# Performance work log

Measured on AMD Instinct MI355X. Metric: run time of the kernel, lower is better.

Reference implementation:

```python
import jax, jax.numpy as jnp
import numpy as np

N_STREAMS = 8
DIM = 1024
N_HEADS = 16
HEAD_DIM = DIM // N_HEADS
STREAM_DIM = DIM // N_STREAMS
EPS = 1e-6


def setup_inputs() -> dict:
    key = jax.random.key(0)
    ks = jax.random.split(key, 20)
    B, S, D = 2, 2048, DIM
    inp = {
        "x": jax.random.normal(ks[0], (B, S, D), jnp.float32),
        "rope_cos": jax.random.uniform(ks[1], (S, HEAD_DIM), jnp.float32),
        "rope_sin": jax.random.uniform(ks[2], (S, HEAD_DIM), jnp.float32),
        # DeltaOperator: learned per-channel decay logits
        "delta_decay": jax.random.normal(ks[3], (D,), jnp.float32) * 0.02,
        # gate_proj: Linear(D, 3*n)
        "gate_w": jax.random.normal(ks[4], (3 * N_STREAMS, D), jnp.float32) * 0.02,
        "gate_b": jnp.zeros((3 * N_STREAMS,), jnp.float32),
        "phi_res": jax.random.normal(ks[5], (N_STREAMS, N_STREAMS), jnp.float32) * 0.02,
        "ln1_w": jnp.ones((D,), jnp.float32),
        "ln2_w": jnp.ones((D,), jnp.float32),
        # MLP (StrategicLinear == Linear at inference)
        "w1": jax.random.normal(ks[6], (4 * D, D), jnp.float32) * 0.02,
        "b1": jnp.zeros((4 * D,), jnp.float32),
        "w2": jax.random.normal(ks[7], (D, 4 * D), jnp.float32) * 0.02,
        "b2": jnp.zeros((D,), jnp.float32),
        # nn.MultiheadAttention params
        "in_proj_w": jax.random.normal(ks[8], (3 * D, D), jnp.float32) * 0.02,
        "in_proj_b": jnp.zeros((3 * D,), jnp.float32),
        "out_w": jax.random.normal(ks[9], (D, D), jnp.float32) * 0.02,
        "out_b": jnp.zeros((D,), jnp.float32),
    }
    return inp


def delta_operator(x, decay_logits):
    # out_t = x_t - s_{t-1};  s_t = beta*s_{t-1} + (1-beta)*x_t  (per-channel EMA delta)
    beta = jax.nn.sigmoid(decay_logits)  # [D]

    def step(s, xt):
        out = xt - s
        s_new = beta * s + (1.0 - beta) * xt
        return s_new, out

    xT = jnp.swapaxes(x, 0, 1)  # [S,B,D]
    s0 = jnp.zeros_like(xT[0])
    _, ysT = jax.lax.scan(step, s0, xT)
    return jnp.swapaxes(ysT, 0, 1)  # [B,S,D]


def rms_norm(x, w):
    var = jnp.mean(x * x, axis=-1, keepdims=True)
    return x * jax.lax.rsqrt(var + EPS) * w


def sinkhorn_knopp(phi, iterations=15):
    K = jnp.exp(phi)
    for _ in range(iterations):
        K = K / jnp.sum(K, axis=1, keepdims=True)
        K = K / jnp.sum(K, axis=0, keepdims=True)
    return K


def causal_mha(x, in_proj_w, in_proj_b, out_w, out_b):
    B, S, D = x.shape
    qkv = x @ in_proj_w.T + in_proj_b  # [B,S,3D]
    q, k, v = jnp.split(qkv, 3, axis=-1)
    def heads(t):
        return t.reshape(B, S, N_HEADS, HEAD_DIM).transpose(0, 2, 1, 3)  # [B,H,S,hd]
    q, k, v = heads(q), heads(k), heads(v)
    scores = jnp.einsum("bhqd,bhkd->bhqk", q, k) / jnp.sqrt(jnp.float32(HEAD_DIM))
    mask = jnp.tril(jnp.ones((S, S), bool))
    scores = jnp.where(mask, scores, jnp.float32(-1e9))
    attn = jax.nn.softmax(scores, axis=-1)
    o = jnp.einsum("bhqk,bhkd->bhqd", attn, v)
    o = o.transpose(0, 2, 1, 3).reshape(B, S, D)
    return o @ out_w.T + out_b


def reference(x, rope_cos, rope_sin, delta_decay, gate_w, gate_b, phi_res,
              ln1_w, ln2_w, w1, b1, w2, b2, in_proj_w, in_proj_b, out_w, out_b):
    B, S, D = x.shape
    n = N_STREAMS
    x_delta = delta_operator(x, delta_decay)
    x_state = jnp.mean(x_delta, axis=1)  # [B,D]
    gates = x_state @ gate_w.T + gate_b  # [B,3n]
    g_res = jax.nn.sigmoid(gates[:, 2 * n:])[:, None, :, None]  # [B,1,n,1]
    H_res = sinkhorn_knopp(phi_res, 15)
    x_streams = x_delta.reshape(B, S, n, STREAM_DIM)
    # (x_perm @ H.T).permute back == einsum over stream axis
    mhc_out = jnp.einsum("bsnd,mn->bsmd", x_streams * g_res, H_res).reshape(B, S, D)
    normed = rms_norm(x_delta, ln1_w)
    attn_out = causal_mha(normed, in_proj_w, in_proj_b, out_w, out_b)
    normed2 = rms_norm(x_delta + attn_out, ln2_w)
    h = jax.nn.gelu(normed2 @ w1.T + b1, approximate=False)
    ffn_out = h @ w2.T + b2
    return x_delta + attn_out + ffn_out + mhc_out
```

## Files before the change

### kernel.cpp

```cpp
#include <hip/hip_runtime.h>
#include <hip/hip_bf16.h>
#include <math.h>

#define BB 2
#define SS 2048
#define DDIM 1024
#define NHEAD 16
#define NSTR 8
#define SDIMC 128
#define NCH 16
#define CLEN 128
#define EPSV 1e-6f

using bf16 = __hip_bfloat16;
typedef __attribute__((ext_vector_type(8))) __bf16 bf8;
typedef __attribute__((ext_vector_type(4))) __bf16 bf4v;
typedef __attribute__((ext_vector_type(4))) float f4;

__device__ __forceinline__ bf16 f2b(float v) { return __float2bfloat16(v); }
__device__ __forceinline__ bf8 ld8(const bf16* p) { return *(const bf8*)p; }
__device__ __forceinline__ f4 MFMA(bf8 a, bf8 b, f4 c) {
  return __builtin_amdgcn_mfma_f32_16x16x32_bf16(a, b, c, 0, 0, 0);
}
__device__ __forceinline__ float sigm(float x) { return 1.0f / (1.0f + expf(-x)); }
__device__ __forceinline__ float fexp2(float x) { return __builtin_amdgcn_exp2f(x); }

__device__ __forceinline__ float gelu_f(float v) {
  float x = v * 0.70710678118654752f;
  float ax = fabsf(x);
  float t = __builtin_amdgcn_rcpf(1.0f + 0.3275911f * ax);
  float p = ((((1.061405429f * t - 1.453152027f) * t + 1.421413741f) * t
              - 0.284496736f) * t + 0.254829592f) * t;
  float e = 1.0f - p * fexp2(-ax * ax * 1.4426950408889634f);
  e = copysignf(e, x);
  return 0.5f * v * (1.0f + e);
}

__device__ __forceinline__ void glds16(bf16* l, const bf16* g) {
  __builtin_amdgcn_global_load_lds(
      (const __attribute__((address_space(1))) unsigned int*)g,
      (__attribute__((address_space(3))) unsigned int*)l, 16, 0, 0);
}

__global__ __launch_bounds__(256) void cvt_all(const float* __restrict__ ipw,
                                               const float* __restrict__ ow,
                                               const float* __restrict__ w1,
                                               const float* __restrict__ w2,
                                               bf16* __restrict__ WIPW,
                                               bf16* __restrict__ WOW,
                                               bf16* __restrict__ W1B,
                                               bf16* __restrict__ W2B) {
  const int S1 = 3 * DDIM * DDIM, S2 = S1 + DDIM * DDIM,
            S3 = S2 + 4 * DDIM * DDIM;
  int i4 = (blockIdx.x * 256 + threadIdx.x) * 4;
  const float* src;
  bf16* dst;
  int off;
  if (i4 < S1)      { src = ipw; dst = WIPW; off = i4; }
  else if (i4 < S2) { src = ow;  dst = WOW;  off = i4 - S1; }
  else if (i4 < S3) { src = w1;  dst = W1B;  off = i4 - S2; }
  else              { src = w2;  dst = W2B;  off = i4 - S3; }
  float4 v = *(const float4*)(src + off);
  bf4v o;
  o[0] = (__bf16)v.x; o[1] = (__bf16)v.y; o[2] = (__bf16)v.z; o[3] = (__bf16)v.w;
  *(bf4v*)(dst + off) = o;
}

__global__ __launch_bounds__(256) void delta_passA(const float* __restrict__ x,
                                                   const float* __restrict__ decay,
                                                   float* __restrict__ SA) {
  int idx = blockIdx.x * 256 + threadIdx.x;
  int d = idx % DDIM;
  int c = (idx / DDIM) % NCH;
  int b = idx / (DDIM * NCH);
  float beta = sigm(decay[d]);
  float omb = 1.0f - beta;
  const float* xp = x + ((size_t)(b * SS + c * CLEN)) * DDIM + d;
  float s = 0.0f;
  for (int j = 0; j < CLEN; j++) {
    float xv = xp[(size_t)j * DDIM];
    s = beta * s + omb * xv;
  }
  SA[idx] = s;
}

__global__ __launch_bounds__(256) void delta_passB(const float* __restrict__ SA,
                                                   const float* __restrict__ decay,
                                                   float* __restrict__ SIN) {
  int idx = blockIdx.x * 256 + threadIdx.x;
  int d = idx % DDIM;
  int b = idx / DDIM;
  float beta = sigm(decay[d]);
  float p = beta;
  for (int i = 0; i < 7; i++) p *= p;
  float s = 0.0f;
  for (int c = 0; c < NCH; c++) {
    SIN[(b * NCH + c) * DDIM + d] = s;
    s = p * s + SA[(b * NCH + c) * DDIM + d];
  }
}

__global__ __launch_bounds__(256) void delta_passC(const float* __restrict__ x,
                                                   const float* __restrict__ decay,
                                                   const float* __restrict__ SIN,
                                                   float* __restrict__ XD,
                                                   float* __restrict__ SA) {
  int idx = blockIdx.x * 256 + threadIdx.x;
  int d = idx % DDIM;
  int c = (idx / DDIM) % NCH;
  int b = idx / (DDIM * NCH);
  float beta = sigm(decay[d]);
  float omb = 1.0f - beta;
  const float* xp = x + ((size_t)(b * SS + c * CLEN)) * DDIM + d;
  float* xdp = XD + ((size_t)(b * SS + c * CLEN)) * DDIM + d;
  float s = SIN[idx];
  float sum = 0.0f;
  for (int j = 0; j < CLEN; j++) {
    float xv = xp[(size_t)j * DDIM];
    float o = xv - s;
    xdp[(size_t)j * DDIM] = o;
    sum += o;
    s = beta * s + omb * xv;
  }
  SA[idx] = sum;
}

__global__ __launch_bounds__(1024) void gates_sinkhorn(const float* __restrict__ SA,
                                                       const float* __restrict__ gw,
                                                       const float* __restrict__ gb,
                                                       const float* __restrict__ phi,
                                                       float* __restrict__ gres,
                                                       float* __restrict__ hres) {
  int tid = threadIdx.x;
  int wave = tid >> 6, lane = tid & 63;
  int b = wave >> 3, j = wave & 7;
  float acc = 0.0f;
  for (int d = lane; d < DDIM; d += 64) {
    float xs = 0.0f;
    for (int c = 0; c < NCH; c++) xs += SA[(b * NCH + c) * DDIM + d];
    xs *= (1.0f / (float)SS);
    acc += xs * gw[(2 * NSTR + j) * DDIM + d];
  }
  for (int off = 32; off > 0; off >>= 1) acc += __shfl_down(acc, off);
  if (lane == 0) gres[b * NSTR + j] = sigm(acc + gb[2 * NSTR + j]);
  __syncthreads();
  if (tid == 0) {
    float Km[8][8];
    for (int i = 0; i < 8; i++)
      for (int jj = 0; jj < 8; jj++) Km[i][jj] = expf(phi[i * 8 + jj]);
    for (int it = 0; it < 15; it++) {
      for (int i = 0; i < 8; i++) {
        float rs = 0.0f;
        for (int jj = 0; jj < 8; jj++) rs += Km[i][jj];
        float inv = 1.0f / rs;
        for (int jj = 0; jj < 8; jj++) Km[i][jj] *= inv;
      }
      for (int jj = 0; jj < 8; jj++) {
        float cs = 0.0f;
        for (int i = 0; i < 8; i++) cs += Km[i][jj];
        float inv = 1.0f / cs;
        for (int i = 0; i < 8; i++) Km[i][jj] *= inv;
      }
    }
    for (int i = 0; i < 8; i++)
      for (int jj = 0; jj < 8; jj++) hres[i * 8 + jj] = Km[i][jj];
  }
}

__global__ __launch_bounds__(256) void rmsnorm_k(const float* __restrict__ in,
                                                 const float* __restrict__ w,
                                                 bf16* __restrict__ out) {
  int row = blockIdx.x;
  const float* r = in + (size_t)row * DDIM;
  int tid = threadIdx.x;
  float ss = 0.0f;
  for (int i = tid; i < DDIM; i += 256) {
    float v = r[i];
    ss += v * v;
  }
  for (int off = 32; off > 0; off >>= 1) ss += __shfl_down(ss, off);
  __shared__ float red[4];
  if ((tid & 63) == 0) red[tid >> 6] = ss;
  __syncthreads();
  float tot = red[0] + red[1] + red[2] + red[3];
  float sc = rsqrtf(tot / (float)DDIM + EPSV);
  bf16* o = out + (size_t)row * DDIM;
  for (int i = tid; i < DDIM; i += 256) o[i] = f2b(r[i] * sc * w[i]);
}

template <int EPI>
__global__ __launch_bounds__(512, 2) void gemm256(const bf16* __restrict__ Ag,
                                                  const bf16* __restrict__ Wg,
                                                  const float* __restrict__ bias,
                                                  bf16* __restrict__ outp,
                                                  int M, int N, int K, int nby) {
  __shared__ __align__(16) bf16 As[2][16384];
  __shared__ __align__(16) bf16 Bs[2][16384];
  int nwg = gridDim.x;
  int cpx = nwg >> 3;
  int l = (blockIdx.x & 7) * cpx + (blockIdx.x >> 3);
  int bm = l / nby, bn = l % nby;
  int m0 = bm * 256, n0 = bn * 256;
  int tid = threadIdx.x;
  int lane = tid & 63, wv = tid >> 6;
  int ml = lane & 15, quad = lane >> 4;
  int wrow = wv >> 2, wcol = wv & 3;

  size_t aoff[2][2], boff[2][2];
  int lof[2][2];
#pragma unroll
  for (int h = 0; h < 2; h++)
#pragma unroll
    for (int j = 0; j < 2; j++) {
      int b = tid * 16 + j * 8192;
      int s = b >> 10, w = b & 1023;
      int wl = w ^ (((w >> 9) & 1) << 5);
      int row = h * 128 + (s >> 1) * 16 + (wl >> 6);
      int col = (s & 1) * 32 + ((wl & 63) >> 1);
      aoff[h][j] = (size_t)(m0 + row) * K + col;
      boff[h][j] = (size_t)(n0 + row) * K + col;
      lof[h][j] = (h * 16384 + b) >> 1;
    }
  int wq2 = ((((ml << 6) + (quad << 4)) ^ (((int)(ml >= 8)) << 5))) >> 1;

#define SA_(c, kt, h) { glds16(&As[c][lof[h][0]], Ag + aoff[h][0] + (size_t)(kt) * 64); \
                        glds16(&As[c][lof[h][1]], Ag + aoff[h][1] + (size_t)(kt) * 64); }
#define SB_(c, kt, h) { glds16(&Bs[c][lof[h][0]], Wg + boff[h][0] + (size_t)(kt) * 64); \
                        glds16(&Bs[c][lof[h][1]], Wg + boff[h][1] + (size_t)(kt) * 64); }

  SA_(0, 0, 0); SA_(0, 0, 1);
  SB_(0, 0, 0); SB_(0, 0, 1);
  SB_(1, 1, 0); SB_(1, 1, 1);
  f4 acc[8][4] = {};
  asm volatile("s_waitcnt vmcnt(4)" ::: "memory");
  __builtin_amdgcn_s_barrier();
  asm volatile("" ::: "memory");

  int T = K >> 6;
  for (int t = 0; t < T; t++) {
    int c = t & 1;
    bf8 bfrag[4][2];
#pragma unroll
    for (int q = 0; q < 4; q++) {
      bf8 af[2][2];
#pragma unroll
      for (int mi2 = 0; mi2 < 2; mi2++)
#pragma unroll
        for (int kk = 0; kk < 2; kk++)
          af[mi2][kk] =
              ld8(&As[c][(((wrow * 8 + q * 2 + mi2) * 2 + kk) << 9) + wq2]);
      if (q == 0) {
#pragma unroll
        for (int ni = 0; ni < 4; ni++)
#pragma unroll
          for (int kk = 0; kk < 2; kk++)
            bfrag[ni][kk] =
                ld8(&Bs[c][(((wcol * 4 + ni) * 2 + kk) << 9) + wq2]);
      }
      if (q == 0 && t + 1 < T) SA_(c ^ 1, t + 1, 0);
      if (q == 1 && t + 1 < T) SA_(c ^ 1, t + 1, 1);
      if (q == 2 && t + 2 < T) SB_(c, t + 2, 0);
      if (q == 3 && t + 2 < T) SB_(c, t + 2, 1);
      __builtin_amdgcn_s_barrier();
      asm volatile("s_waitcnt lgkmcnt(0)" ::: "memory");
      __builtin_amdgcn_s_setprio(1);
#pragma unroll
      for (int mi2 = 0; mi2 < 2; mi2++)
#pragma unroll
        for (int ni = 0; ni < 4; ni++)
#pragma unroll
          for (int kk = 0; kk < 2; kk++)
            acc[q * 2 + mi2][ni] =
                MFMA(af[mi2][kk], bfrag[ni][kk], acc[q * 2 + mi2][ni]);
      __builtin_amdgcn_s_setprio(0);
      if (q == 3) {
        if (t + 2 < T) {
          asm volatile("s_waitcnt vmcnt(4)" ::: "memory");
        } else if (t + 1 < T) {
          asm volatile("s_waitcnt vmcnt(0)" ::: "memory");
        }
      }
      __builtin_amdgcn_s_barrier();
      asm volatile("" ::: "memory");
    }
  }
#pragma unroll
  for (int mi = 0; mi < 8; mi++)
#pragma unroll
    for (int ni = 0; ni < 4; ni++)
#pragma unroll
      for (int r = 0; r < 4; r++) {
        int row = m0 + wrow * 128 + mi * 16 + quad * 4 + r;
        int col = n0 + wcol * 64 + ni * 16 + ml;
        float v = acc[mi][ni][r] + bias[col];
        if (EPI == 1) v = gelu_f(v);
        outp[(size_t)row * N + col] = f2b(v);
      }
#undef SA_
#undef SB_
}

__global__ __launch_bounds__(256) void gemm_part2(const bf16* __restrict__ A,
                                                  const bf16* __restrict__ W,
                                                  float* __restrict__ P0,
                                                  float* __restrict__ P1,
                                                  int M, int N, int KS, int LDK) {
  __shared__ bf16 As[2][128 * 32];
  __shared__ bf16 Bs[2][128 * 32];
  int tid = threadIdx.x;
  int lane = tid & 63, wv = tid >> 6;
  int ml = lane & 15, quad = lane >> 4;
  int wr = wv >> 1, wc = wv & 1;
  int m0 = blockIdx.x * 128, n0 = blockIdx.y * 128;
  const bf16* Ab = A + blockIdx.z * KS;
  const bf16* Wb = W + blockIdx.z * KS;
  float* P = blockIdx.z ? P1 : P0;
  const bf16* ga[2];
  const bf16* gb[2];
  int lofs[2];
#pragma unroll
  for (int it = 0; it < 2; it++) {
    int c = it * 256 + tid;
    int row = c >> 2, kc = (c & 3) * 8;
    ga[it] = Ab + (size_t)(m0 + row) * LDK + kc;
    gb[it] = Wb + (size_t)(n0 + row) * LDK + kc;
    lofs[it] = c * 8;
  }
#pragma unroll
  for (int it = 0; it < 2; it++) {
    glds16(&As[0][lofs[it]], ga[it]);
    glds16(&Bs[0][lofs[it]], gb[it]);
  }
  f4 acc[4][4] = {};
  int nk = KS >> 5;
  int cur = 0;
  __syncthreads();
  for (int t = 0; t < nk; t++) {
    if (t + 1 < nk) {
      int ko = (t + 1) * 32;
#pragma unroll
      for (int it = 0; it < 2; it++) {
        glds16(&As[cur ^ 1][lofs[it]], ga[it] + ko);
        glds16(&Bs[cur ^ 1][lofs[it]], gb[it] + ko);
      }
    }
    bf8 af[4], bfr[4];
#pragma unroll
    for (int mi = 0; mi < 4; mi++)
      af[mi] = ld8(&As[cur][(wr * 64 + mi * 16 + ml) * 32 + quad * 8]);
#pragma unroll
    for (int ni = 0; ni < 4; ni++)
      bfr[ni] = ld8(&Bs[cur][(wc * 64 + ni * 16 + ml) * 32 + quad * 8]);
#pragma unroll
    for (int mi = 0; mi < 4; mi++)
#pragma unroll
      for (int ni = 0; ni < 4; ni++)
        acc[mi][ni] = MFMA(af[mi], bfr[ni], acc[mi][ni]);
    __syncthreads();
    cur ^= 1;
  }
#pragma unroll
  for (int mi = 0; mi < 4; mi++)
#pragma unroll
    for (int ni = 0; ni < 4; ni++)
#pragma unroll
      for (int r = 0; r < 4; r++) {
        int row = m0 + wr * 64 + mi * 16 + quad * 4 + r;
        int col = n0 + wc * 64 + ni * 16 + ml;
        P[(size_t)row * N + col] = acc[mi][ni][r];
      }
}

template <int ODT, int EPI>
__global__ __launch_bounds__(256) void gemm_lds64(const bf16* __restrict__ A,
                                                  const bf16* __restrict__ W,
                                                  const float* __restrict__ bias,
                                                  const float* __restrict__ res,
                                                  void* __restrict__ outp,
                                                  int M, int N, int K) {
  __shared__ bf16 As[2][64 * 32];
  __shared__ bf16 Bs[2][128 * 32];
  int tid = threadIdx.x;
  int lane = tid & 63, wv = tid >> 6;
  int ml = lane & 15, quad = lane >> 4;
  int wr = wv & 1, wc = wv >> 1;
  int m0 = blockIdx.x * 64, n0 = blockIdx.y * 128;
  const bf16* gaA;
  const bf16* gb[2];
  int lofA, lofs[2];
  {
    int c = tid;
    int row = c >> 2, kc = (c & 3) * 8;
    gaA = A + (size_t)(m0 + row) * K + kc;
    lofA = c * 8;
  }
#pragma unroll
  for (int it = 0; it < 2; it++) {
    int c = it * 256 + tid;
    int row = c >> 2, kc = (c & 3) * 8;
    gb[it] = W + (size_t)(n0 + row) * K + kc;
    lofs[it] = c * 8;
  }
  glds16(&As[0][lofA], gaA);
#pragma unroll
  for (int it = 0; it < 2; it++) glds16(&Bs[0][lofs[it]], gb[it]);
  f4 acc[2][4] = {};
  int nk = K >> 5;
  int cur = 0;
  __syncthreads();
  for (int t = 0; t < nk; t++) {
    if (t + 1 < nk) {
      int ko = (t + 1) * 32;
      glds16(&As[cur ^ 1][lofA], gaA + ko);
#pragma unroll
      for (int it = 0; it < 2; it++) glds16(&Bs[cur ^ 1][lofs[it]], gb[it] + ko);
    }
    bf8 af[2], bfr[4];
#pragma unroll
    for (int mi = 0; mi < 2; mi++)
      af[mi] = ld8(&As[cur][(wr * 32 + mi * 16 + ml) * 32 + quad * 8]);
#pragma unroll
    for (int ni = 0; ni < 4; ni++)
      bfr[ni] = ld8(&Bs[cur][(wc * 64 + ni * 16 + ml) * 32 + quad * 8]);
#pragma unroll
    for (int mi = 0; mi < 2; mi++)
#pragma unroll
      for (int ni = 0; ni < 4; ni++)
        acc[mi][ni] = MFMA(af[mi], bfr[ni], acc[mi][ni]);
    __syncthreads();
    cur ^= 1;
  }
#pragma unroll
  for (int mi = 0; mi < 2; mi++)
#pragma unroll
    for (int ni = 0; ni < 4; ni++)
#pragma unroll
      for (int r = 0; r < 4; r++) {
        int row = m0 + wr * 32 + mi * 16 + quad * 4 + r;
        int col = n0 + wc * 64 + ni * 16 + ml;
        size_t idx = (size_t)row * N + col;
        float v = acc[mi][ni][r] + bias[col];
        if (EPI == 1) v = gelu_f(v);
        if (EPI == 2) v += res[idx];
        if (ODT == 1) ((bf16*)outp)[idx] = f2b(v);
        else ((float*)outp)[idx] = v;
      }
}

__global__ __launch_bounds__(256) void vtrans(const bf16* __restrict__ qkv,
                                              bf16* __restrict__ VT) {
  int bid = blockIdx.x;
  int st = bid % (SS / 64);
  int h = (bid / (SS / 64)) % NHEAD;
  int b = bid / ((SS / 64) * NHEAD);
  __shared__ bf16 tile[64][65];
  int s0 = st * 64;
  int tid = threadIdx.x;
  for (int it = 0; it < 16; it++) {
    int sl = it * 4 + (tid >> 6), dl = tid & 63;
    tile[sl][dl] = qkv[(size_t)(b * SS + s0 + sl) * (3 * DDIM) + 2 * DDIM + h * 64 + dl];
  }
  __syncthreads();
  for (int it = 0; it < 16; it++) {
    int dl = it * 4 + (tid >> 6), sl = tid & 63;
    VT[((size_t)(b * NHEAD + h) * 64 + dl) * SS + s0 + sl] = tile[sl][dl];
  }
}

__device__ __forceinline__ void qk_softmax(bool active, int kt, int q0, int nkt,
                                           const bf8 kf[4][2], const bf8* qf,
                                           f4* oacc, float& m, float& l,
                                           bf8* pf, bf16 (*pl)[72],
                                           int ml, int quad, int k0) {
  if (!active) return;
  const float SC = 0.125f * 1.44269504089f;
  f4 s[4] = {{0,0,0,0},{0,0,0,0},{0,0,0,0},{0,0,0,0}};
  __builtin_amdgcn_s_setprio(1);
#pragma unroll
  for (int kk = 0; kk < 2; kk++)
#pragma unroll
    for (int c = 0; c < 4; c++)
      s[c] = MFMA(kf[c][kk], qf[kk], s[c]);
  __builtin_amdgcn_s_setprio(0);
  if (kt == nkt - 1) {
    int qi = q0 + ml;
#pragma unroll
    for (int c = 0; c < 4; c++)
#pragma unroll
      for (int r = 0; r < 4; r++)
        if (k0 + c * 16 + quad * 4 + r > qi) s[c][r] = -1e30f;
  }
  float mx = s[0][0];
#pragma unroll
  for (int c = 0; c < 4; c++)
#pragma unroll
    for (int r = 0; r < 4; r++) mx = fmaxf(mx, s[c][r]);
  mx = fmaxf(mx, __shfl_xor(mx, 16));
  mx = fmaxf(mx, __shfl_xor(mx, 32));
  float mn = fmaxf(m, mx * SC);
  float alpha = fexp2(m - mn);
  float rs = 0.0f;
  float p[4][4];
#pragma unroll
  for (int c = 0; c < 4; c++)
#pragma unroll
    for (int r = 0; r < 4; r++) {
      p[c][r] = fexp2(__builtin_fmaf(s[c][r], SC, -mn));
      rs += p[c][r];
    }
  rs += __shfl_xor(rs, 16);
  rs += __shfl_xor(rs, 32);
  l = l * alpha + rs;
  m = mn;
  float alr[4];
#pragma unroll
  for (int r = 0; r < 4; r++) alr[r] = __shfl(alpha, quad * 4 + r);
#pragma unroll
  for (int c = 0; c < 4; c++)
#pragma unroll
    for (int r = 0; r < 4; r++) oacc[c][r] *= alr[r];
#pragma unroll
  for (int c = 0; c < 4; c++) {
    bf4v w;
#pragma unroll
    for (int r = 0; r < 4; r++) w[r] = (__bf16)p[c][r];
    *(bf4v*)&pl[ml][c * 16 + quad * 4] = w;
  }
#pragma unroll
  for (int kk = 0; kk < 2; kk++) pf[kk] = ld8(&pl[ml][kk * 32 + quad * 8]);
}

__device__ __forceinline__ void pv_acc(bool active, const bf8* pf,
                                       const bf8 vf[4][2], f4* oacc) {
  if (!active) return;
  __builtin_amdgcn_s_setprio(1);
#pragma unroll
  for (int c = 0; c < 4; c++)
#pragma unroll
    for (int kk = 0; kk < 2; kk++)
      oacc[c] = MFMA(pf[kk], vf[c][kk], oacc[c]);
  __builtin_amdgcn_s_setprio(0);
}

__global__ __launch_bounds__(256) void flash_attn(const bf16* __restrict__ qkv,
                                                  const bf16* __restrict__ VT,
                                                  bf16* __restrict__ obuf) {
  int rb = blockIdx.x;
  int bid = (rb & 7) * 64 + (rb >> 3);
  int j = bid & 15;
  int blk = (j & 1) ? (15 - (j >> 1)) : (j >> 1);
  int h = (bid >> 4) & 15;
  int b = bid >> 8;
  int tid = threadIdx.x;
  int wv = tid >> 6, lane = tid & 63;
  int ml = lane & 15, quad = lane >> 4;
  int idx0 = blk * 4 + wv;
  int idx1 = 127 - idx0;
  int q0a = idx0 * 16, q0b = idx1 * 16;
  int nkt0 = blk + 1;
  int nkt1 = 32 - blk;
  int maxn = nkt1;

  __shared__ __align__(16) bf16 Ks[2][64 * 64];
  __shared__ __align__(16) bf16 Vs[2][64 * 64];
  __shared__ __align__(16) bf16 plds[4][2][16][72];
  bf16 (*plA)[72] = plds[wv][0];
  bf16 (*plB)[72] = plds[wv][1];

  bf8 qfa[2], qfb[2];
#pragma unroll
  for (int kk = 0; kk < 2; kk++) {
    qfa[kk] = ld8(qkv + (size_t)(b * SS + q0a + ml) * (3 * DDIM) + h * 64 + kk * 32 + quad * 8);
    qfb[kk] = ld8(qkv + (size_t)(b * SS + q0b + ml) * (3 * DDIM) + h * 64 + kk * 32 + quad * 8);
  }
  f4 oacca[4] = {{0,0,0,0},{0,0,0,0},{0,0,0,0},{0,0,0,0}};
  f4 oaccb[4] = {{0,0,0,0},{0,0,0,0},{0,0,0,0},{0,0,0,0}};
  float ma = -1e30f, la = 0.0f, mb = -1e30f, lb = 0.0f;

  const bf16* kglob = qkv + (size_t)b * SS * (3 * DDIM) + DDIM + h * 64;
  const bf16* vglob = VT + (size_t)(b * NHEAD + h) * 64 * SS;

#pragma unroll
  for (int it = 0; it < 2; it++) {
    int lam = it * 256 + tid;
    int row = lam >> 3;
    int ch = (lam & 7) ^ (row & 7);
    glds16(&Ks[0][lam * 8], kglob + (size_t)row * (3 * DDIM) + ch * 8);
    glds16(&Vs[0][lam * 8], vglob + (size_t)row * SS + ch * 8);
  }
  __syncthreads();
  int cur = 0;
  for (int kt = 0; kt < maxn; kt++) {
    int k0 = kt * 64;
    if (kt + 1 < maxn) {
      int k0n = (kt + 1) * 64;
#pragma unroll
      for (int it = 0; it < 2; it++) {
        int lam = it * 256 + tid;
        int row = lam >> 3;
        int ch = (lam & 7) ^ (row & 7);
        glds16(&Ks[cur ^ 1][lam * 8], kglob + (size_t)(k0n + row) * (3 * DDIM) + ch * 8);
        glds16(&Vs[cur ^ 1][lam * 8], vglob + (size_t)row * SS + k0n + ch * 8);
      }
    }
    bool act0 = kt < nkt0;
    bf8 kf[4][2];
#pragma unroll
    for (int kk = 0; kk < 2; kk++)
#pragma unroll
      for (int c = 0; c < 4; c++) {
        int chunk = ((c * 16 + ml) << 3) + ((kk * 4 + quad) ^ (ml & 7));
        kf[c][kk] = ld8(&Ks[cur][chunk * 8]);
      }
    bf8 pfa[2], pfb[2];
    qk_softmax(act0, kt, q0a, nkt0, kf, qfa, oacca, ma, la, pfa, plA, ml, quad, k0);
    qk_softmax(true, kt, q0b, nkt1, kf, qfb, oaccb, mb, lb, pfb, plB, ml, quad, k0);
    bf8 vf[4][2];
#pragma unroll
    for (int kk = 0; kk < 2; kk++)
#pragma unroll
      for (int c = 0; c < 4; c++) {
        int chunk = ((c * 16 + ml) << 3) + ((kk * 4 + quad) ^ (ml & 7));
        vf[c][kk] = ld8(&Vs[cur][chunk * 8]);
      }
    pv_acc(act0, pfa, vf, oacca);
    pv_acc(true, pfb, vf, oaccb);
    __syncthreads();
    cur ^= 1;
  }
  float lna[4], lnb[4];
#pragma unroll
  for (int r = 0; r < 4; r++) {
    lna[r] = __shfl(la, quad * 4 + r);
    lnb[r] = __shfl(lb, quad * 4 + r);
  }
#pragma unroll
  for (int c = 0; c < 4; c++)
#pragma unroll
    for (int r = 0; r < 4; r++) {
      int rowa = q0a + quad * 4 + r;
      int rowb = q0b + quad * 4 + r;
      obuf[(size_t)(b * SS + rowa) * DDIM + h * 64 + c * 16 + ml] =
          f2b(oacca[c][r] / lna[r]);
      obuf[(size_t)(b * SS + rowb) * DDIM + h * 64 + c * 16 + ml] =
          f2b(oaccb[c][r] / lnb[r]);
    }
}

__global__ __launch_bounds__(256) void final_k(const float* __restrict__ y,
                                               const float* __restrict__ P0,
                                               const float* __restrict__ P1,
                                               const float* __restrict__ bias,
                                               const float* __restrict__ xd,
                                               const float* __restrict__ hres,
                                               const float* __restrict__ gres,
                                               float* __restrict__ out) {
  int row = blockIdx.x;
  int b = row / SS;
  int tid = threadIdx.x;
  __shared__ float cf[8][8];
  if (tid < 64) cf[tid >> 3][tid & 7] = hres[tid] * gres[b * NSTR + (tid & 7)];
  __syncthreads();
  const float* yr = y + (size_t)row * DDIM;
  const float* p0 = P0 + (size_t)row * DDIM;
  const float* p1 = P1 + (size_t)row * DDIM;
  const float* xr = xd + (size_t)row * DDIM;
  float* o = out + (size_t)row * DDIM;
  for (int i = tid; i < DDIM; i += 256) {
    int m = i >> 7, dd = i & 127;
    float acc = yr[i] + p0[i] + p1[i] + bias[i];
#pragma unroll
    for (int n = 0; n < 8; n++) acc += cf[m][n] * xr[n * SDIMC + dd];
    o[i] = acc;
  }
}

extern "C" void kernel_launch(void* const* d_in, const int* in_sizes, int n_in,
                              void* d_out, int out_size, void* d_ws, size_t ws_size,
                              hipStream_t stream) {
  const float* x     = (const float*)d_in[0];
  const float* decay = (const float*)d_in[3];
  const float* gw    = (const float*)d_in[4];
  const float* gb    = (const float*)d_in[5];
  const float* phi   = (const float*)d_in[6];
  const float* ln1   = (const float*)d_in[7];
  const float* ln2   = (const float*)d_in[8];
  const float* w1    = (const float*)d_in[9];
  const float* b1    = (const float*)d_in[10];
  const float* w2    = (const float*)d_in[11];
  const float* b2    = (const float*)d_in[12];
  const float* ipw   = (const float*)d_in[13];
  const float* ipb   = (const float*)d_in[14];
  const float* ow    = (const float*)d_in[15];
  const float* obs   = (const float*)d_in[16];
  float* out = (float*)d_out;

  const size_t MB = 1048576ull;
  char* wsp = (char*)d_ws;
  float* SA   = (float*)(wsp);
  float* SIN  = (float*)(wsp + 131072ull);
  float* GRES = (float*)(wsp + 262144ull);
  float* HRES = (float*)(wsp + 262208ull);
  float* XD   = (float*)(wsp + 1 * MB);
  float* AO   = (float*)(wsp + 17 * MB);
  bf16*  NORM = (bf16*)(wsp + 33 * MB);
  bf16*  OB   = (bf16*)(wsp + 41 * MB);
  bf16*  QKV  = (bf16*)(wsp + 49 * MB);
  bf16*  VT   = (bf16*)(wsp + 73 * MB);
  bf16*  HB   = (bf16*)(wsp + 49 * MB);
  bf16*  WIPW = (bf16*)(wsp + 81 * MB);
  bf16*  WOW  = (bf16*)(wsp + 87 * MB);
  bf16*  W1B  = (bf16*)(wsp + 89 * MB);
  bf16*  W2B  = (bf16*)(wsp + 97 * MB);
  float* PK0  = (float*)(wsp + 33 * MB);
  float* PK1  = (float*)(wsp + 81 * MB);

  cvt_all<<<dim3(12 * DDIM * DDIM / 1024), dim3(256), 0, stream>>>(
      ipw, ow, w1, w2, WIPW, WOW, W1B, W2B);

  delta_passA<<<dim3(BB * NCH * DDIM / 256), dim3(256), 0, stream>>>(x, decay, SA);
  delta_passB<<<dim3(BB * DDIM / 256), dim3(256), 0, stream>>>(SA, decay, SIN);
  delta_passC<<<dim3(BB * NCH * DDIM / 256), dim3(256), 0, stream>>>(x, decay, SIN, XD, SA);
  gates_sinkhorn<<<dim3(1), dim3(1024), 0, stream>>>(SA, gw, gb, phi, GRES, HRES);
  rmsnorm_k<<<dim3(BB * SS), dim3(256), 0, stream>>>(XD, ln1, NORM);
  gemm256<0><<<dim3(192), dim3(512), 0, stream>>>(NORM, WIPW, ipb, QKV,
                                                  BB * SS, 3 * DDIM, DDIM, 12);
  vtrans<<<dim3(BB * NHEAD * (SS / 64)), dim3(256), 0, stream>>>(QKV, VT);
  flash_attn<<<dim3(BB * NHEAD * 16), dim3(256), 0, stream>>>(QKV, VT, OB);
  gemm_lds64<0, 2><<<dim3(64, 8), dim3(256), 0, stream>>>(OB, WOW, obs, XD,
                                                          AO, BB * SS, DDIM, DDIM);
  rmsnorm_k<<<dim3(BB * SS), dim3(256), 0, stream>>>(AO, ln2, NORM);
  gemm256<1><<<dim3(256), dim3(512), 0, stream>>>(NORM, W1B, b1, HB,
                                                  BB * SS, 4 * DDIM, DDIM, 16);
  gemm_part2<<<dim3(32, 8, 2), dim3(256), 0, stream>>>(HB, W2B, PK0, PK1,
                                                       BB * SS, DDIM, 2 * DDIM, 4 * DDIM);
  final_k<<<dim3(BB * SS), dim3(256), 0, stream>>>(AO, PK0, PK1, b2, XD,
                                                   HRES, GRES, out);
}
```

Before: 417.4 us.

## Use 256x256 split-K GEMM for FFN down-proj, lazy softmax rescale, vectorize final

Replaces the 128x128 two-way split-K down-projection GEMM with a 256x256-tile, 512-thread kernel split four ways along K. It uses swizzled LDS staging, an XCD-aware block remap, and bf16 partial outputs. The final combine kernel now reads four bf16 partials with vectorized float4 loads. Flash attention skips the max update and accumulator rescale when the new block max exceeds the running max by at most 8 (log2 units), and uses 3-way max chains. Storing the partials in bf16 costs some precision, and the lazy rescale lets softmax terms grow to about 2^8 before a rescale happens.

```diff
diff --git a/kernel.cpp b/kernel.cpp
--- a/kernel.cpp
+++ b/kernel.cpp
@@ -24,6 +24,9 @@
 }
 __device__ __forceinline__ float sigm(float x) { return 1.0f / (1.0f + expf(-x)); }
 __device__ __forceinline__ float fexp2(float x) { return __builtin_amdgcn_exp2f(x); }
+__device__ __forceinline__ float max3f(float a, float b, float c) {
+  return fmaxf(fmaxf(a, b), c);
+}
 
 __device__ __forceinline__ float gelu_f(float v) {
   float x = v * 0.70710678118654752f;
@@ -300,75 +303,120 @@
 #undef SB_
 }
 
-__global__ __launch_bounds__(256) void gemm_part2(const bf16* __restrict__ A,
-                                                  const bf16* __restrict__ W,
-                                                  float* __restrict__ P0,
-                                                  float* __restrict__ P1,
-                                                  int M, int N, int KS, int LDK) {
-  __shared__ bf16 As[2][128 * 32];
-  __shared__ bf16 Bs[2][128 * 32];
+__global__ __launch_bounds__(512, 2) void gemm256sk(const bf16* __restrict__ Ag,
+                                                    const bf16* __restrict__ Wg,
+                                                    bf16* __restrict__ P01,
+                                                    bf16* __restrict__ P23,
+                                                    int M, int N, int K, int LDK,
+                                                    int nby) {
+  __shared__ __align__(16) bf16 As[2][16384];
+  __shared__ __align__(16) bf16 Bs[2][16384];
+  int nwg = gridDim.x;
+  int cpx = nwg >> 3;
+  int l = (blockIdx.x & 7) * cpx + (blockIdx.x >> 3);
+  int nper = nwg >> 2;
+  int sk = l / nper;
+  int idx = l % nper;
+  int bm = idx / nby, bn = idx % nby;
+  int m0 = bm * 256, n0 = bn * 256;
+  bf16* outp = (sk < 2) ? (P01 + (size_t)sk * M * N)
+                        : (P23 + (size_t)(sk - 2) * M * N);
+  int kbase = sk * K;
   int tid = threadIdx.x;
   int lane = tid & 63, wv = tid >> 6;
   int ml = lane & 15, quad = lane >> 4;
-  int wr = wv >> 1, wc = wv & 1;
-  int m0 = blockIdx.x * 128, n0 = blockIdx.y * 128;
-  const bf16* Ab = A + blockIdx.z * KS;
-  const bf16* Wb = W + blockIdx.z * KS;
-  float* P = blockIdx.z ? P1 : P0;
-  const bf16* ga[2];
-  const bf16* gb[2];
-  int lofs[2];
-#pragma unroll
-  for (int it = 0; it < 2; it++) {
-    int c = it * 256 + tid;
-    int row = c >> 2, kc = (c & 3) * 8;
-    ga[it] = Ab + (size_t)(m0 + row) * LDK + kc;
-    gb[it] = Wb + (size_t)(n0 + row) * LDK + kc;
-    lofs[it] = c * 8;
-  }
-#pragma unroll
-  for (int it = 0; it < 2; it++) {
-    glds16(&As[0][lofs[it]], ga[it]);
-    glds16(&Bs[0][lofs[it]], gb[it]);
-  }
-  f4 acc[4][4] = {};
-  int nk = KS >> 5;
-  int cur = 0;
-  __syncthreads();
-  for (int t = 0; t < nk; t++) {
-    if (t + 1 < nk) {
-      int ko = (t + 1) * 32;
-#pragma unroll
-      for (int it = 0; it < 2; it++) {
-        glds16(&As[cur ^ 1][lofs[it]], ga[it] + ko);
-        glds16(&Bs[cur ^ 1][lofs[it]], gb[it] + ko);
-      }
+  int wrow = wv >> 2, wcol = wv & 3;
+
+  size_t aoff[2][2], boff[2][2];
+  int lof[2][2];
+#pragma unroll
+  for (int h = 0; h < 2; h++)
+#pragma unroll
+    for (int j = 0; j < 2; j++) {
+      int b = tid * 16 + j * 8192;
+      int s = b >> 10, w = b & 1023;
+      int wl = w ^ (((w >> 9) & 1) << 5);
+      int row = h * 128 + (s >> 1) * 16 + (wl >> 6);
+      int col = (s & 1) * 32 + ((wl & 63) >> 1);
+      aoff[h][j] = (size_t)(m0 + row) * LDK + kbase + col;
+      boff[h][j] = (size_t)(n0 + row) * LDK + kbase + col;
+      lof[h][j] = (h * 16384 + b) >> 1;
     }
-    bf8 af[4], bfr[4];
-#pragma unroll
-    for (int mi = 0; mi < 4; mi++)
-      af[mi] = ld8(&As[cur][(wr * 64 + mi * 16 + ml) * 32 + quad * 8]);
+  int wq2 = ((((ml << 6) + (quad << 4)) ^ (((int)(ml >= 8)) << 5))) >> 1;
+
+#define SA_(c, kt, h) { glds16(&As[c][lof[h][0]], Ag + aoff[h][0] + (size_t)(kt) * 64); \
+                        glds16(&As[c][lof[h][1]], Ag + aoff[h][1] + (size_t)(kt) * 64); }
+#define SB_(c, kt, h) { glds16(&Bs[c][lof[h][0]], Wg + boff[h][0] + (size_t)(kt) * 64); \
+                        glds16(&Bs[c][lof[h][1]], Wg + boff[h][1] + (size_t)(kt) * 64); }
+
+  SA_(0, 0, 0); SA_(0, 0, 1);
+  SB_(0, 0, 0); SB_(0, 0, 1);
+  SB_(1, 1, 0); SB_(1, 1, 1);
+  f4 acc[8][4] = {};
+  asm volatile("s_waitcnt vmcnt(4)" ::: "memory");
+  __builtin_amdgcn_s_barrier();
+  asm volatile("" ::: "memory");
+
+  int T = K >> 6;
+  for (int t = 0; t < T; t++) {
+    int c = t & 1;
+    bf8 bfrag[4][2];
+#pragma unroll
+    for (int q = 0; q < 4; q++) {
+      bf8 af[2][2];
+#pragma unroll
+      for (int mi2 = 0; mi2 < 2; mi2++)
+#pragma unroll
+        for (int kk = 0; kk < 2; kk++)
+          af[mi2][kk] =
+              ld8(&As[c][(((wrow * 8 + q * 2 + mi2) * 2 + kk) << 9) + wq2]);
+      if (q == 0) {
+#pragma unroll
+        for (int ni = 0; ni < 4; ni++)
+#pragma unroll
+          for (int kk = 0; kk < 2; kk++)
+            bfrag[ni][kk] =
+                ld8(&Bs[c][(((wcol * 4 + ni) * 2 + kk) << 9) + wq2]);
+      }
+      if (q == 0 && t + 1 < T) SA_(c ^ 1, t + 1, 0);
+      if (q == 1 && t + 1 < T) SA_(c ^ 1, t + 1, 1);
+      if (q == 2 && t + 2 < T) SB_(c, t + 2, 0);
+      if (q == 3 && t + 2 < T) SB_(c, t + 2, 1);
+      __builtin_amdgcn_s_barrier();
+      asm volatile("s_waitcnt lgkmcnt(0)" ::: "memory");
+      __builtin_amdgcn_s_setprio(1);
+#pragma unroll
+      for (int mi2 = 0; mi2 < 2; mi2++)
+#pragma unroll
+        for (int ni = 0; ni < 4; ni++)
+#pragma unroll
+          for (int kk = 0; kk < 2; kk++)
+            acc[q * 2 + mi2][ni] =
+                MFMA(af[mi2][kk], bfrag[ni][kk], acc[q * 2 + mi2][ni]);
+      __builtin_amdgcn_s_setprio(0);
+      if (q == 3) {
+        if (t + 2 < T) {
+          asm volatile("s_waitcnt vmcnt(4)" ::: "memory");
+        } else if (t + 1 < T) {
+          asm volatile("s_waitcnt vmcnt(0)" ::: "memory");
+        }
+      }
+      __builtin_amdgcn_s_barrier();
+      asm volatile("" ::: "memory");
+    }
+  }
+#pragma unroll
+  for (int mi = 0; mi < 8; mi++)
 #pragma unroll
     for (int ni = 0; ni < 4; ni++)
-      bfr[ni] = ld8(&Bs[cur][(wc * 64 + ni * 16 + ml) * 32 + quad * 8]);
-#pragma unroll
-    for (int mi = 0; mi < 4; mi++)
-#pragma unroll
-      for (int ni = 0; ni < 4; ni++)
-        acc[mi][ni] = MFMA(af[mi], bfr[ni], acc[mi][ni]);
-    __syncthreads();
-    cur ^= 1;
-  }
-#pragma unroll
-  for (int mi = 0; mi < 4; mi++)
-#pragma unroll
-    for (int ni = 0; ni < 4; ni++)
 #pragma unroll
       for (int r = 0; r < 4; r++) {
-        int row = m0 + wr * 64 + mi * 16 + quad * 4 + r;
-        int col = n0 + wc * 64 + ni * 16 + ml;
-        P[(size_t)row * N + col] = acc[mi][ni][r];
-      }
+        int row = m0 + wrow * 128 + mi * 16 + quad * 4 + r;
+        int col = n0 + wcol * 64 + ni * 16 + ml;
+        outp[(size_t)row * N + col] = f2b(acc[mi][ni][r]);
+      }
+#undef SA_
+#undef SB_
 }
 
 template <int ODT, int EPI>
@@ -490,35 +538,52 @@
       for (int r = 0; r < 4; r++)
         if (k0 + c * 16 + quad * 4 + r > qi) s[c][r] = -1e30f;
   }
-  float mx = s[0][0];
-#pragma unroll
-  for (int c = 0; c < 4; c++)
-#pragma unroll
-    for (int r = 0; r < 4; r++) mx = fmaxf(mx, s[c][r]);
+  float mx = max3f(s[0][0], s[0][1], s[0][2]);
+  mx = max3f(mx, s[0][3], s[1][0]);
+  mx = max3f(mx, s[1][1], s[1][2]);
+  mx = max3f(mx, s[1][3], s[2][0]);
+  mx = max3f(mx, s[2][1], s[2][2]);
+  mx = max3f(mx, s[2][3], s[3][0]);
+  mx = max3f(mx, s[3][1], s[3][2]);
+  mx = fmaxf(mx, s[3][3]);
   mx = fmaxf(mx, __shfl_xor(mx, 16));
   mx = fmaxf(mx, __shfl_xor(mx, 32));
-  float mn = fmaxf(m, mx * SC);
-  float alpha = fexp2(m - mn);
+  float mxs = mx * SC;
+  float p[4][4];
   float rs = 0.0f;
-  float p[4][4];
-#pragma unroll
-  for (int c = 0; c < 4; c++)
-#pragma unroll
-    for (int r = 0; r < 4; r++) {
-      p[c][r] = fexp2(__builtin_fmaf(s[c][r], SC, -mn));
-      rs += p[c][r];
-    }
-  rs += __shfl_xor(rs, 16);
-  rs += __shfl_xor(rs, 32);
-  l = l * alpha + rs;
-  m = mn;
-  float alr[4];
-#pragma unroll
-  for (int r = 0; r < 4; r++) alr[r] = __shfl(alpha, quad * 4 + r);
-#pragma unroll
-  for (int c = 0; c < 4; c++)
-#pragma unroll
-    for (int r = 0; r < 4; r++) oacc[c][r] *= alr[r];
+  if (__all(mxs - m <= 8.0f)) {
+#pragma unroll
+    for (int c = 0; c < 4; c++)
+#pragma unroll
+      for (int r = 0; r < 4; r++) {
+        p[c][r] = fexp2(__builtin_fmaf(s[c][r], SC, -m));
+        rs += p[c][r];
+      }
+    rs += __shfl_xor(rs, 16);
+    rs += __shfl_xor(rs, 32);
+    l += rs;
+  } else {
+    float mn = fmaxf(m, mxs);
+    float alpha = fexp2(m - mn);
+#pragma unroll
+    for (int c = 0; c < 4; c++)
+#pragma unroll
+      for (int r = 0; r < 4; r++) {
+        p[c][r] = fexp2(__builtin_fmaf(s[c][r], SC, -mn));
+        rs += p[c][r];
+      }
+    rs += __shfl_xor(rs, 16);
+    rs += __shfl_xor(rs, 32);
+    l = l * alpha + rs;
+    m = mn;
+    float alr[4];
+#pragma unroll
+    for (int r = 0; r < 4; r++) alr[r] = __shfl(alpha, quad * 4 + r);
+#pragma unroll
+    for (int c = 0; c < 4; c++)
+#pragma unroll
+      for (int r = 0; r < 4; r++) oacc[c][r] *= alr[r];
+  }
 #pragma unroll
   for (int c = 0; c < 4; c++) {
     bf4v w;
@@ -648,8 +713,10 @@
 }
 
 __global__ __launch_bounds__(256) void final_k(const float* __restrict__ y,
-                                               const float* __restrict__ P0,
-                                               const float* __restrict__ P1,
+                                               const bf16* __restrict__ P0,
+                                               const bf16* __restrict__ P1,
+                                               const bf16* __restrict__ P2,
+                                               const bf16* __restrict__ P3,
                                                const float* __restrict__ bias,
                                                const float* __restrict__ xd,
                                                const float* __restrict__ hres,
@@ -661,18 +728,29 @@
   __shared__ float cf[8][8];
   if (tid < 64) cf[tid >> 3][tid & 7] = hres[tid] * gres[b * NSTR + (tid & 7)];
   __syncthreads();
-  const float* yr = y + (size_t)row * DDIM;
-  const float* p0 = P0 + (size_t)row * DDIM;
-  const float* p1 = P1 + (size_t)row * DDIM;
+  int i4 = tid * 4;
+  int m = i4 >> 7, dd = i4 & 127;
+  size_t base = (size_t)row * DDIM + i4;
+  f4 vy = *(const f4*)(y + base);
+  f4 vb = *(const f4*)(bias + i4);
+  bf4v p0 = *(const bf4v*)(P0 + base);
+  bf4v p1 = *(const bf4v*)(P1 + base);
+  bf4v p2 = *(const bf4v*)(P2 + base);
+  bf4v p3 = *(const bf4v*)(P3 + base);
   const float* xr = xd + (size_t)row * DDIM;
-  float* o = out + (size_t)row * DDIM;
-  for (int i = tid; i < DDIM; i += 256) {
-    int m = i >> 7, dd = i & 127;
-    float acc = yr[i] + p0[i] + p1[i] + bias[i];
-#pragma unroll
-    for (int n = 0; n < 8; n++) acc += cf[m][n] * xr[n * SDIMC + dd];
-    o[i] = acc;
-  }
+  float acc[4];
+#pragma unroll
+  for (int jj = 0; jj < 4; jj++)
+    acc[jj] = vy[jj] + vb[jj] + (float)p0[jj] + (float)p1[jj] +
+              (float)p2[jj] + (float)p3[jj];
+#pragma unroll
+  for (int n = 0; n < 8; n++) {
+    f4 vx = *(const f4*)(xr + n * SDIMC + dd);
+#pragma unroll
+    for (int jj = 0; jj < 4; jj++) acc[jj] += cf[m][n] * vx[jj];
+  }
+  f4 vo = {acc[0], acc[1], acc[2], acc[3]};
+  *(f4*)(out + base) = vo;
 }
 
 extern "C" void kernel_launch(void* const* d_in, const int* in_sizes, int n_in,
@@ -712,8 +790,8 @@
   bf16*  WOW  = (bf16*)(wsp + 87 * MB);
   bf16*  W1B  = (bf16*)(wsp + 89 * MB);
   bf16*  W2B  = (bf16*)(wsp + 97 * MB);
-  float* PK0  = (float*)(wsp + 33 * MB);
-  float* PK1  = (float*)(wsp + 81 * MB);
+  bf16* PKB0 = (bf16*)(wsp + 33 * MB);
+  bf16* PKB2 = (bf16*)(wsp + 81 * MB);
 
   cvt_all<<<dim3(12 * DDIM * DDIM / 1024), dim3(256), 0, stream>>>(
       ipw, ow, w1, w2, WIPW, WOW, W1B, W2B);
@@ -732,8 +810,9 @@
   rmsnorm_k<<<dim3(BB * SS), dim3(256), 0, stream>>>(AO, ln2, NORM);
   gemm256<1><<<dim3(256), dim3(512), 0, stream>>>(NORM, W1B, b1, HB,
                                                   BB * SS, 4 * DDIM, DDIM, 16);
-  gemm_part2<<<dim3(32, 8, 2), dim3(256), 0, stream>>>(HB, W2B, PK0, PK1,
-                                                       BB * SS, DDIM, 2 * DDIM, 4 * DDIM);
-  final_k<<<dim3(BB * SS), dim3(256), 0, stream>>>(AO, PK0, PK1, b2, XD,
-                                                   HRES, GRES, out);
-}
+  gemm256sk<<<dim3(256), dim3(512), 0, stream>>>(HB, W2B, PKB0, PKB2,
+                                                 BB * SS, DDIM, DDIM, 4 * DDIM, 4);
+  final_k<<<dim3(BB * SS), dim3(256), 0, stream>>>(
+      AO, PKB0, PKB0 + (size_t)BB * SS * DDIM, PKB2,
+      PKB2 + (size_t)BB * SS * DDIM, b2, XD, HRES, GRES, out);
+}
```

Result: faster. 395.8 us (-5.2%).
